# Kernel optimization log

Hardware: AMD Instinct MI355X
Metric: run time of the kernel (lower is better)

The kernel has to match this reference:

```python
import jax, jax.numpy as jnp
import numpy as np

INPUT_SIZE = 128
OUTPUT_SIZE = 32
LIFTING_DIM = 512
BATCH = 32768


def setup_inputs() -> dict:
    key = jax.random.key(0)
    ks = jax.random.split(key, 7)
    x = jax.random.normal(ks[0], (BATCH, INPUT_SIZE), dtype=jnp.float32)
    # Linear(input_size, lifting_dim) with bias (torch layout: W [out, in])
    lim1 = 1.0 / np.sqrt(INPUT_SIZE)
    W1 = jax.random.uniform(ks[1], (LIFTING_DIM, INPUT_SIZE), jnp.float32, -lim1, lim1)
    b1 = jax.random.uniform(ks[2], (LIFTING_DIM,), jnp.float32, -lim1, lim1)
    # Linear(lifting_dim, output_size, bias=False)
    lim2 = 1.0 / np.sqrt(LIFTING_DIM)
    W2 = jax.random.uniform(ks[3], (OUTPUT_SIZE, LIFTING_DIM), jnp.float32, -lim2, lim2)
    # Quadratic params: L_vars ~ randn, b ~ randn, c ~ randn (as in module init)
    n_tril = LIFTING_DIM * (LIFTING_DIM + 1) // 2
    L_vars = jax.random.normal(ks[4], (n_tril,), dtype=jnp.float32)
    qb = jax.random.normal(ks[5], (LIFTING_DIM,), dtype=jnp.float32)
    qc = jax.random.normal(ks[6], (1,), dtype=jnp.float32)
    return {"x": x, "W1": W1, "b1": b1, "W2": W2, "L_vars": L_vars, "qb": qb, "qc": qc}


def reference(x, W1, b1, W2, L_vars, qb, qc):
    # lifting: phi = tanh(x @ W1^T + b1)   [B, lifting_dim]
    phi = jnp.tanh(x @ W1.T + b1)
    # actor: linear feedback (no bias)     [B, output_size]
    pi = phi @ W2.T
    # critic: quadratic form y = phi' Q phi + b' phi + c with Q = L L^T (PSD)
    rows, cols = jnp.tril_indices(LIFTING_DIM)  # row-major, same order as torch.tril_indices
    L = jnp.zeros((LIFTING_DIM, LIFTING_DIM), dtype=L_vars.dtype).at[rows, cols].set(L_vars)
    Q = L @ L.T
    # diag(phi @ Q @ phi.T) == sum((phi @ Q) * phi, axis=1)  -- O(B*d^2), same math
    y = jnp.sum((phi @ Q) * phi, axis=1) + phi @ qb + qc  # [B]
    vf = y[:, None]  # [B, 1]
    return pi, vf
```

## Files before the change

### kernel.cpp

```cpp
#include <hip/hip_runtime.h>
#include <hip/hip_bf16.h>
#include <stdint.h>

typedef short bf16x8 __attribute__((ext_vector_type(8)));
typedef float f32x4 __attribute__((ext_vector_type(4)));

#define DEVI static __device__ __forceinline__

constexpr int B_   = 32768;
constexpr int IN_  = 128;
constexpr int LF_  = 512;
constexpr int OUT_ = 32;

constexpr size_t OFF_LTF = 0;
constexpr size_t OFF_W1F = 524288;
constexpr size_t OFF_W2F = OFF_W1F + 131072;

DEVI short f2bs(float f) { __hip_bfloat16 h = __float2bfloat16(f); return *(short*)&h; }

DEVI float tanh_fast(float v) {
    float e = __expf(2.0f * v);
    return 1.0f - 2.0f * __builtin_amdgcn_rcpf(e + 1.0f);
}

DEVI bf16x8 fragGL(const __hip_bfloat16* base, int chunk, int ln) {
    return *(const bf16x8*)(base + ((size_t)chunk * 64 + ln) * 8);
}

DEVI bf16x8 phiFrag(const char* p, int row, int kofs) {
    int c = (kofs >> 3) ^ (row & 7);
    return *(const bf16x8*)(p + (size_t)((row << 6) + c) * 16);
}
DEVI bf16x8 xFrag(const char* p, int row, int kofs) {
    int c = (kofs >> 3) ^ (row & 15);
    return *(const bf16x8*)(p + (size_t)((row << 4) + c) * 16);
}

__global__ __launch_bounds__(256) void k_prep(
        const float* __restrict__ w1, const float* __restrict__ w2,
        const float* __restrict__ lv, const float* __restrict__ qb,
        __hip_bfloat16* __restrict__ w1f, __hip_bfloat16* __restrict__ w2f,
        __hip_bfloat16* __restrict__ ltf) {
    int cid = blockIdx.x * 256 + threadIdx.x;
    if (cid < 8192) {
        int ln = cid & 63, ks = (cid >> 6) & 3, nt = cid >> 8;
        int n = nt * 16 + (ln & 15), kb = ks * 32 + (ln >> 4) * 8;
        const float* src = w1 + (size_t)n * IN_ + kb;
        bf16x8 o;
#pragma unroll
        for (int i = 0; i < 8; ++i) o[i] = f2bs(src[i]);
        *(bf16x8*)(w1f + (size_t)cid * 8) = o;
    } else if (cid < 11264) {
        int c2 = cid - 8192;
        int ln = c2 & 63, ks = (c2 >> 6) & 15, nt = c2 >> 10;
        int n = nt * 16 + (ln & 15), kb = ks * 32 + (ln >> 4) * 8;
        bf16x8 o;
#pragma unroll
        for (int i = 0; i < 8; ++i) {
            float v = (n < OUT_) ? w2[(size_t)n * LF_ + kb + i]
                                 : (n == OUT_ ? qb[kb + i] : 0.f);
            o[i] = f2bs(v);
        }
        *(bf16x8*)(w2f + (size_t)c2 * 8) = o;
    } else if (cid < 44032) {
        int c3 = cid - 11264;
        int ln = c3 & 63, ks = (c3 >> 6) & 15, t = c3 >> 10;
        int j = t * 16 + (ln & 15), kb = ks * 32 + (ln >> 4) * 8;
        bf16x8 o;
#pragma unroll
        for (int i = 0; i < 8; ++i) {
            int k = kb + i;
            o[i] = (k >= j) ? f2bs(lv[(size_t)k * (k + 1) / 2 + j]) : (short)0;
        }
        *(bf16x8*)(ltf + (size_t)c3 * 8) = o;
    }
}

__global__ __launch_bounds__(512, 4) void k_fused(
        const float* __restrict__ x, const __hip_bfloat16* __restrict__ w1f,
        const float* __restrict__ b1, const __hip_bfloat16* __restrict__ w2f,
        const __hip_bfloat16* __restrict__ ltf, const float* __restrict__ qcp,
        float* __restrict__ pi, float* __restrict__ vf) {
    __shared__ char smem[81920];
    char*  phiB  = smem;
    char*  stage = smem + 65536;
    float* vfb   = (float*)stage;
    float* vfp   = (float*)(stage + 256);

    const int tid = threadIdx.x, wv = tid >> 6, ln = tid & 63;
    const int cl = ln & 15, q = ln >> 4;
    const int m0 = blockIdx.x * 64;

#pragma unroll
    for (int it = 0; it < 2; ++it) {
        int slot = it * 512 + tid, row = slot >> 4, cg = slot & 15;
        const float4* p = (const float4*)(x + (size_t)(m0 + row) * IN_ + cg * 8);
        float4 u0 = p[0], u1 = p[1];
        bf16x8 pk;
        pk[0] = f2bs(u0.x); pk[1] = f2bs(u0.y); pk[2] = f2bs(u0.z); pk[3] = f2bs(u0.w);
        pk[4] = f2bs(u1.x); pk[5] = f2bs(u1.y); pk[6] = f2bs(u1.z); pk[7] = f2bs(u1.w);
        *(bf16x8*)(stage + (size_t)((row << 4) + (cg ^ (row & 15))) * 16) = pk;
    }
    __syncthreads();

    {
        f32x4 acc[4][4] = {};
        bf16x8 wfr[4], wnx[4];
#pragma unroll
        for (int ni = 0; ni < 4; ++ni) wfr[ni] = fragGL(w1f, (4 * wv + ni) * 4, ln);
#pragma unroll
        for (int ks = 0; ks < 4; ++ks) {
            bf16x8 a[4];
#pragma unroll
            for (int mi = 0; mi < 4; ++mi) a[mi] = xFrag(stage, mi * 16 + cl, ks * 32 + q * 8);
            if (ks < 3)
#pragma unroll
                for (int ni = 0; ni < 4; ++ni)
                    wnx[ni] = fragGL(w1f, (4 * wv + ni) * 4 + ks + 1, ln);
#pragma unroll
            for (int ni = 0; ni < 4; ++ni)
#pragma unroll
                for (int mi = 0; mi < 4; ++mi)
                    acc[ni][mi] = __builtin_amdgcn_mfma_f32_16x16x32_bf16(
                        wfr[ni], a[mi], acc[ni][mi], 0, 0, 0);
#pragma unroll
            for (int ni = 0; ni < 4; ++ni) wfr[ni] = wnx[ni];
        }
#pragma unroll
        for (int ni = 0; ni < 4; ++ni) {
            float4 bb = *(const float4*)(b1 + wv * 64 + ni * 16 + q * 4);
            int c0 = wv * 8 + ni * 2 + (q >> 1);
#pragma unroll
            for (int mi = 0; mi < 4; ++mi) {
                int row = mi * 16 + cl;
                short4 pk;
                pk.x = f2bs(tanh_fast(acc[ni][mi][0] + bb.x));
                pk.y = f2bs(tanh_fast(acc[ni][mi][1] + bb.y));
                pk.z = f2bs(tanh_fast(acc[ni][mi][2] + bb.z));
                pk.w = f2bs(tanh_fast(acc[ni][mi][3] + bb.w));
                *(short4*)(phiB + (size_t)((row << 6) + (c0 ^ (row & 7))) * 16
                           + (q & 1) * 8) = pk;
            }
        }
    }
    __syncthreads();

    {
        int ids[2] = { (wv < 4) ? 2 * wv : 8 + (wv - 4), (wv < 4) ? 2 * wv + 1 : -1 };
#pragma unroll
        for (int u = 0; u < 2; ++u) {
            int id = ids[u];
            if (id < 0) continue;
            int mi = id & 3, ni = id >> 2;
            f32x4 a2 = {};
#pragma unroll
            for (int ks = 0; ks < 16; ++ks) {
                bf16x8 a = phiFrag(phiB, mi * 16 + cl, ks * 32 + q * 8);
                bf16x8 b = fragGL(w2f, ni * 16 + ks, ln);
                a2 = __builtin_amdgcn_mfma_f32_16x16x32_bf16(a, b, a2, 0, 0, 0);
            }
#pragma unroll
            for (int r = 0; r < 4; ++r) {
                int row = mi * 16 + q * 4 + r, col = ni * 16 + cl;
                if (col < OUT_)       pi[(size_t)(m0 + row) * OUT_ + col] = a2[r];
                else if (col == OUT_) vfb[row] = a2[r];
            }
        }
    }

    {
        const int tl[4] = { wv, 15 - wv, 16 + wv, 31 - wv };
        int kstart[4];
#pragma unroll
        for (int j = 0; j < 4; ++j) kstart[j] = (tl[j] * 16) & ~31;
        const int kmin = kstart[0];
        f32x4 acc[4][4] = {};
        bf16x8 b[4];
#pragma unroll
        for (int j = 0; j < 4; ++j)
            if (kmin >= kstart[j]) b[j] = fragGL(ltf, tl[j] * 16 + (kmin >> 5), ln);
        for (int k0 = kmin; k0 < LF_; k0 += 32) {
            int k1 = k0 + 32;
            bf16x8 a[4];
#pragma unroll
            for (int mi = 0; mi < 4; ++mi) a[mi] = phiFrag(phiB, mi * 16 + cl, k0 + q * 8);
            bf16x8 bn[4];
            if (k1 < LF_) {
                int ks1 = k1 >> 5;
#pragma unroll
                for (int j = 0; j < 4; ++j)
                    if (k1 >= kstart[j]) bn[j] = fragGL(ltf, tl[j] * 16 + ks1, ln);
            }
#pragma unroll
            for (int j = 0; j < 4; ++j) {
                if (k0 >= kstart[j]) {
#pragma unroll
                    for (int mi = 0; mi < 4; ++mi)
                        acc[j][mi] = __builtin_amdgcn_mfma_f32_16x16x32_bf16(
                            a[mi], b[j], acc[j][mi], 0, 0, 0);
                }
            }
#pragma unroll
            for (int j = 0; j < 4; ++j) b[j] = bn[j];
        }
#pragma unroll
        for (int mi = 0; mi < 4; ++mi)
#pragma unroll
            for (int r = 0; r < 4; ++r) {
                float s = 0.f;
#pragma unroll
                for (int j = 0; j < 4; ++j) { float t = acc[j][mi][r]; s += t * t; }
                s += __shfl_xor(s, 1, 64);
                s += __shfl_xor(s, 2, 64);
                s += __shfl_xor(s, 4, 64);
                s += __shfl_xor(s, 8, 64);
                if (cl == 0) vfp[wv * 64 + mi * 16 + q * 4 + r] = s;
            }
    }
    __syncthreads();
    if (tid < 64) {
        float v = vfb[tid] + qcp[0];
#pragma unroll
        for (int w = 0; w < 8; ++w) v += vfp[w * 64 + tid];
        vf[m0 + tid] = v;
    }
}

extern "C" void kernel_launch(void* const* d_in, const int* in_sizes, int n_in,
                              void* d_out, int out_size, void* d_ws, size_t ws_size,
                              hipStream_t stream) {
    const float* x  = (const float*)d_in[0];
    const float* w1 = (const float*)d_in[1];
    const float* b1 = (const float*)d_in[2];
    const float* w2 = (const float*)d_in[3];
    const float* lv = (const float*)d_in[4];
    const float* qb = (const float*)d_in[5];
    const float* qc = (const float*)d_in[6];

    char* ws = (char*)d_ws;
    __hip_bfloat16* ltf = (__hip_bfloat16*)(ws + OFF_LTF);
    __hip_bfloat16* w1f = (__hip_bfloat16*)(ws + OFF_W1F);
    __hip_bfloat16* w2f = (__hip_bfloat16*)(ws + OFF_W2F);

    float* pi = (float*)d_out;
    float* vf = pi + (size_t)B_ * OUT_;

    k_prep <<<172, 256, 0, stream>>>(w1, w2, lv, qb, w1f, w2f, ltf);
    k_fused<<<B_ / 64, 512, 0, stream>>>(x, w1f, b1, w2f, ltf, qc, pi, vf);
}
```

Measured before the change: 108.6 us.

## Switch quadratic-form GEMM to 32x32x16 MFMA with per-wave templated triangular loops

The L-factor GEMM in the critic path now uses 32x32x16 bf16 MFMA tiles instead of 16x16x32. Each wave takes two 32-column tiles of L, paired so the triangular work is balanced, and runs fully unrolled compile-time loops chosen through a switch on the wave index. The L prep layout is reworked to match the 32-wide fragments, and the reduction shuffles widen to 32 lanes. The register prefetch of W1 fragments in the first GEMM is also dropped in favour of loading them inside each k-step, which may expose global load latency.

```diff
diff --git a/kernel.cpp b/kernel.cpp
--- a/kernel.cpp
+++ b/kernel.cpp
@@ -4,6 +4,7 @@
 
 typedef short bf16x8 __attribute__((ext_vector_type(8)));
 typedef float f32x4 __attribute__((ext_vector_type(4)));
+typedef float f32x16 __attribute__((ext_vector_type(16)));
 
 #define DEVI static __device__ __forceinline__
 
@@ -26,14 +27,47 @@
 DEVI bf16x8 fragGL(const __hip_bfloat16* base, int chunk, int ln) {
     return *(const bf16x8*)(base + ((size_t)chunk * 64 + ln) * 8);
 }
+DEVI f32x16 mfma32(bf16x8 a, bf16x8 b, f32x16 c) {
+    return __builtin_amdgcn_mfma_f32_32x32x16_bf16(a, b, c, 0, 0, 0);
+}
 
 DEVI bf16x8 phiFrag(const char* p, int row, int kofs) {
     int c = (kofs >> 3) ^ (row & 7);
     return *(const bf16x8*)(p + (size_t)((row << 6) + c) * 16);
 }
+DEVI bf16x8 phiFrag32(const char* p, int h, int ks, int ln) {
+    int row = h * 32 + (ln & 31);
+    int c = (ks * 2 + (ln >> 5)) ^ (row & 7);
+    return *(const bf16x8*)(p + (size_t)((row << 6) + c) * 16);
+}
 DEVI bf16x8 xFrag(const char* p, int row, int kofs) {
     int c = (kofs >> 3) ^ (row & 15);
     return *(const bf16x8*)(p + (size_t)((row << 4) + c) * 16);
+}
+
+template <int WV>
+DEVI void p3loops(const char* phiB, const __hip_bfloat16* ltf, int ln,
+                  f32x16 acc[2][2]) {
+    constexpr int T1 = 15 - WV;
+#pragma unroll
+    for (int ks = 2 * WV; ks < 2 * T1; ++ks) {
+        bf16x8 b0 = fragGL(ltf, WV * 32 + ks, ln);
+        bf16x8 a0 = phiFrag32(phiB, 0, ks, ln);
+        bf16x8 a1 = phiFrag32(phiB, 1, ks, ln);
+        acc[0][0] = mfma32(a0, b0, acc[0][0]);
+        acc[0][1] = mfma32(a1, b0, acc[0][1]);
+    }
+#pragma unroll
+    for (int ks = 2 * T1; ks < 32; ++ks) {
+        bf16x8 b0 = fragGL(ltf, WV * 32 + ks, ln);
+        bf16x8 b1 = fragGL(ltf, T1 * 32 + ks, ln);
+        bf16x8 a0 = phiFrag32(phiB, 0, ks, ln);
+        bf16x8 a1 = phiFrag32(phiB, 1, ks, ln);
+        acc[0][0] = mfma32(a0, b0, acc[0][0]);
+        acc[0][1] = mfma32(a1, b0, acc[0][1]);
+        acc[1][0] = mfma32(a0, b1, acc[1][0]);
+        acc[1][1] = mfma32(a1, b1, acc[1][1]);
+    }
 }
 
 __global__ __launch_bounds__(256) void k_prep(
@@ -64,13 +98,13 @@
         *(bf16x8*)(w2f + (size_t)c2 * 8) = o;
     } else if (cid < 44032) {
         int c3 = cid - 11264;
-        int ln = c3 & 63, ks = (c3 >> 6) & 15, t = c3 >> 10;
-        int j = t * 16 + (ln & 15), kb = ks * 32 + (ln >> 4) * 8;
+        int ln = c3 & 63, ks = (c3 >> 6) & 31, t = c3 >> 11;
+        int n = t * 32 + (ln & 31), kb = ks * 16 + (ln >> 5) * 8;
         bf16x8 o;
 #pragma unroll
         for (int i = 0; i < 8; ++i) {
             int k = kb + i;
-            o[i] = (k >= j) ? f2bs(lv[(size_t)k * (k + 1) / 2 + j]) : (short)0;
+            o[i] = (k >= n) ? f2bs(lv[(size_t)k * (k + 1) / 2 + n]) : (short)0;
         }
         *(bf16x8*)(ltf + (size_t)c3 * 8) = o;
     }
@@ -105,26 +139,19 @@
 
     {
         f32x4 acc[4][4] = {};
-        bf16x8 wfr[4], wnx[4];
-#pragma unroll
-        for (int ni = 0; ni < 4; ++ni) wfr[ni] = fragGL(w1f, (4 * wv + ni) * 4, ln);
 #pragma unroll
         for (int ks = 0; ks < 4; ++ks) {
-            bf16x8 a[4];
+            bf16x8 a[4], wfr[4];
 #pragma unroll
             for (int mi = 0; mi < 4; ++mi) a[mi] = xFrag(stage, mi * 16 + cl, ks * 32 + q * 8);
-            if (ks < 3)
-#pragma unroll
-                for (int ni = 0; ni < 4; ++ni)
-                    wnx[ni] = fragGL(w1f, (4 * wv + ni) * 4 + ks + 1, ln);
+#pragma unroll
+            for (int ni = 0; ni < 4; ++ni) wfr[ni] = fragGL(w1f, (4 * wv + ni) * 4 + ks, ln);
 #pragma unroll
             for (int ni = 0; ni < 4; ++ni)
 #pragma unroll
                 for (int mi = 0; mi < 4; ++mi)
                     acc[ni][mi] = __builtin_amdgcn_mfma_f32_16x16x32_bf16(
                         wfr[ni], a[mi], acc[ni][mi], 0, 0, 0);
-#pragma unroll
-            for (int ni = 0; ni < 4; ++ni) wfr[ni] = wnx[ni];
         }
 #pragma unroll
         for (int ni = 0; ni < 4; ++ni) {
@@ -169,52 +196,30 @@
     }
 
     {
-        const int tl[4] = { wv, 15 - wv, 16 + wv, 31 - wv };
-        int kstart[4];
-#pragma unroll
-        for (int j = 0; j < 4; ++j) kstart[j] = (tl[j] * 16) & ~31;
-        const int kmin = kstart[0];
-        f32x4 acc[4][4] = {};
-        bf16x8 b[4];
-#pragma unroll
-        for (int j = 0; j < 4; ++j)
-            if (kmin >= kstart[j]) b[j] = fragGL(ltf, tl[j] * 16 + (kmin >> 5), ln);
-        for (int k0 = kmin; k0 < LF_; k0 += 32) {
-            int k1 = k0 + 32;
-            bf16x8 a[4];
-#pragma unroll
-            for (int mi = 0; mi < 4; ++mi) a[mi] = phiFrag(phiB, mi * 16 + cl, k0 + q * 8);
-            bf16x8 bn[4];
-            if (k1 < LF_) {
-                int ks1 = k1 >> 5;
-#pragma unroll
-                for (int j = 0; j < 4; ++j)
-                    if (k1 >= kstart[j]) bn[j] = fragGL(ltf, tl[j] * 16 + ks1, ln);
-            }
-#pragma unroll
-            for (int j = 0; j < 4; ++j) {
-                if (k0 >= kstart[j]) {
-#pragma unroll
-                    for (int mi = 0; mi < 4; ++mi)
-                        acc[j][mi] = __builtin_amdgcn_mfma_f32_16x16x32_bf16(
-                            a[mi], b[j], acc[j][mi], 0, 0, 0);
-                }
-            }
-#pragma unroll
-            for (int j = 0; j < 4; ++j) b[j] = bn[j];
-        }
-#pragma unroll
-        for (int mi = 0; mi < 4; ++mi)
-#pragma unroll
-            for (int r = 0; r < 4; ++r) {
-                float s = 0.f;
-#pragma unroll
-                for (int j = 0; j < 4; ++j) { float t = acc[j][mi][r]; s += t * t; }
+        f32x16 acc[2][2] = {};
+        switch (wv) {
+            case 0: p3loops<0>(phiB, ltf, ln, acc); break;
+            case 1: p3loops<1>(phiB, ltf, ln, acc); break;
+            case 2: p3loops<2>(phiB, ltf, ln, acc); break;
+            case 3: p3loops<3>(phiB, ltf, ln, acc); break;
+            case 4: p3loops<4>(phiB, ltf, ln, acc); break;
+            case 5: p3loops<5>(phiB, ltf, ln, acc); break;
+            case 6: p3loops<6>(phiB, ltf, ln, acc); break;
+            default: p3loops<7>(phiB, ltf, ln, acc); break;
+        }
+#pragma unroll
+        for (int h = 0; h < 2; ++h)
+#pragma unroll
+            for (int r = 0; r < 16; ++r) {
+                float t0 = acc[0][h][r], t1 = acc[1][h][r];
+                float s = t0 * t0 + t1 * t1;
                 s += __shfl_xor(s, 1, 64);
                 s += __shfl_xor(s, 2, 64);
                 s += __shfl_xor(s, 4, 64);
                 s += __shfl_xor(s, 8, 64);
-                if (cl == 0) vfp[wv * 64 + mi * 16 + q * 4 + r] = s;
+                s += __shfl_xor(s, 16, 64);
+                if ((ln & 31) == 0)
+                    vfp[wv * 64 + h * 32 + (r & 3) + 8 * (r >> 2) + 4 * (ln >> 5)] = s;
             }
     }
     __syncthreads();
```

Result: no change. 108.7 us (+0.1%).

## Use slab-based phi LDS layout, drop register prefetch, reorder actor after critic

Applied to the files above, without the earlier changes.

Phi is now stored in shared memory in a per-slab chunked layout that matches the MFMA fragment order, replacing the XOR-swizzled row layout, so fragment loads become contiguous 16-byte slot accesses. The explicit double-buffered global prefetch of W1 and L fragments is removed in favour of direct loads inside the loop, which lowers register pressure but relies on the compiler and occupancy to hide latency. The actor (W2) matmul is moved after the critic quadratic-form stage.

```diff
diff --git a/kernel.cpp b/kernel.cpp
--- a/kernel.cpp
+++ b/kernel.cpp
@@ -26,14 +26,18 @@
 DEVI bf16x8 fragGL(const __hip_bfloat16* base, int chunk, int ln) {
     return *(const bf16x8*)(base + ((size_t)chunk * 64 + ln) * 8);
 }
-
-DEVI bf16x8 phiFrag(const char* p, int row, int kofs) {
-    int c = (kofs >> 3) ^ (row & 7);
-    return *(const bf16x8*)(p + (size_t)((row << 6) + c) * 16);
-}
+DEVI f32x4 mfma16(bf16x8 a, bf16x8 b, f32x4 c) {
+    return __builtin_amdgcn_mfma_f32_16x16x32_bf16(a, b, c, 0, 0, 0);
+}
+
 DEVI bf16x8 xFrag(const char* p, int row, int kofs) {
     int c = (kofs >> 3) ^ (row & 15);
     return *(const bf16x8*)(p + (size_t)((row << 4) + c) * 16);
+}
+DEVI bf16x8 phi16s(const char* slab, int mi, int ksl, int cl, int q) {
+    int chunk = ksl * 4 + (q >> 1) * 2 + (mi >> 1);
+    int slot  = (mi & 1) * 16 + cl + 32 * (q & 1);
+    return *(const bf16x8*)(slab + ((size_t)chunk * 64 + slot) * 16);
 }
 
 __global__ __launch_bounds__(256) void k_prep(
@@ -82,7 +86,7 @@
         const __hip_bfloat16* __restrict__ ltf, const float* __restrict__ qcp,
         float* __restrict__ pi, float* __restrict__ vf) {
     __shared__ char smem[81920];
-    char*  phiB  = smem;
+    char*  phiS  = smem;
     char*  stage = smem + 65536;
     float* vfb   = (float*)stage;
     float* vfp   = (float*)(stage + 256);
@@ -105,68 +109,39 @@
 
     {
         f32x4 acc[4][4] = {};
-        bf16x8 wfr[4], wnx[4];
-#pragma unroll
-        for (int ni = 0; ni < 4; ++ni) wfr[ni] = fragGL(w1f, (4 * wv + ni) * 4, ln);
 #pragma unroll
         for (int ks = 0; ks < 4; ++ks) {
-            bf16x8 a[4];
+            bf16x8 a[4], wfr[4];
 #pragma unroll
             for (int mi = 0; mi < 4; ++mi) a[mi] = xFrag(stage, mi * 16 + cl, ks * 32 + q * 8);
-            if (ks < 3)
-#pragma unroll
-                for (int ni = 0; ni < 4; ++ni)
-                    wnx[ni] = fragGL(w1f, (4 * wv + ni) * 4 + ks + 1, ln);
+#pragma unroll
+            for (int ni = 0; ni < 4; ++ni) wfr[ni] = fragGL(w1f, (4 * wv + ni) * 4 + ks, ln);
 #pragma unroll
             for (int ni = 0; ni < 4; ++ni)
 #pragma unroll
                 for (int mi = 0; mi < 4; ++mi)
                     acc[ni][mi] = __builtin_amdgcn_mfma_f32_16x16x32_bf16(
                         wfr[ni], a[mi], acc[ni][mi], 0, 0, 0);
-#pragma unroll
-            for (int ni = 0; ni < 4; ++ni) wfr[ni] = wnx[ni];
-        }
+        }
+        char* slab = phiS + (size_t)(wv >> 1) * 16384;
 #pragma unroll
         for (int ni = 0; ni < 4; ++ni) {
             float4 bb = *(const float4*)(b1 + wv * 64 + ni * 16 + q * 4);
-            int c0 = wv * 8 + ni * 2 + (q >> 1);
+            int chunk = (wv & 1) * 8 + ni * 2;
 #pragma unroll
             for (int mi = 0; mi < 4; ++mi) {
-                int row = mi * 16 + cl;
                 short4 pk;
                 pk.x = f2bs(tanh_fast(acc[ni][mi][0] + bb.x));
                 pk.y = f2bs(tanh_fast(acc[ni][mi][1] + bb.y));
                 pk.z = f2bs(tanh_fast(acc[ni][mi][2] + bb.z));
                 pk.w = f2bs(tanh_fast(acc[ni][mi][3] + bb.w));
-                *(short4*)(phiB + (size_t)((row << 6) + (c0 ^ (row & 7))) * 16
+                int slot = (mi & 1) * 16 + cl + 32 * (q >> 1);
+                *(short4*)(slab + ((size_t)(chunk + (mi >> 1)) * 64 + slot) * 16
                            + (q & 1) * 8) = pk;
             }
         }
     }
     __syncthreads();
-
-    {
-        int ids[2] = { (wv < 4) ? 2 * wv : 8 + (wv - 4), (wv < 4) ? 2 * wv + 1 : -1 };
-#pragma unroll
-        for (int u = 0; u < 2; ++u) {
-            int id = ids[u];
-            if (id < 0) continue;
-            int mi = id & 3, ni = id >> 2;
-            f32x4 a2 = {};
-#pragma unroll
-            for (int ks = 0; ks < 16; ++ks) {
-                bf16x8 a = phiFrag(phiB, mi * 16 + cl, ks * 32 + q * 8);
-                bf16x8 b = fragGL(w2f, ni * 16 + ks, ln);
-                a2 = __builtin_amdgcn_mfma_f32_16x16x32_bf16(a, b, a2, 0, 0, 0);
-            }
-#pragma unroll
-            for (int r = 0; r < 4; ++r) {
-                int row = mi * 16 + q * 4 + r, col = ni * 16 + cl;
-                if (col < OUT_)       pi[(size_t)(m0 + row) * OUT_ + col] = a2[r];
-                else if (col == OUT_) vfb[row] = a2[r];
-            }
-        }
-    }
 
     {
         const int tl[4] = { wv, 15 - wv, 16 + wv, 31 - wv };
@@ -175,33 +150,23 @@
         for (int j = 0; j < 4; ++j) kstart[j] = (tl[j] * 16) & ~31;
         const int kmin = kstart[0];
         f32x4 acc[4][4] = {};
-        bf16x8 b[4];
-#pragma unroll
-        for (int j = 0; j < 4; ++j)
-            if (kmin >= kstart[j]) b[j] = fragGL(ltf, tl[j] * 16 + (kmin >> 5), ln);
         for (int k0 = kmin; k0 < LF_; k0 += 32) {
-            int k1 = k0 + 32;
+            int ks = k0 >> 5;
+            const char* slab = phiS + (size_t)(ks >> 2) * 16384;
+            int ksl = ks & 3;
             bf16x8 a[4];
 #pragma unroll
-            for (int mi = 0; mi < 4; ++mi) a[mi] = phiFrag(phiB, mi * 16 + cl, k0 + q * 8);
-            bf16x8 bn[4];
-            if (k1 < LF_) {
-                int ks1 = k1 >> 5;
-#pragma unroll
-                for (int j = 0; j < 4; ++j)
-                    if (k1 >= kstart[j]) bn[j] = fragGL(ltf, tl[j] * 16 + ks1, ln);
-            }
+            for (int mi = 0; mi < 4; ++mi) a[mi] = phi16s(slab, mi, ksl, cl, q);
 #pragma unroll
             for (int j = 0; j < 4; ++j) {
                 if (k0 >= kstart[j]) {
+                    bf16x8 b = fragGL(ltf, tl[j] * 16 + ks, ln);
 #pragma unroll
                     for (int mi = 0; mi < 4; ++mi)
                         acc[j][mi] = __builtin_amdgcn_mfma_f32_16x16x32_bf16(
-                            a[mi], b[j], acc[j][mi], 0, 0, 0);
+                            a[mi], b, acc[j][mi], 0, 0, 0);
                 }
             }
-#pragma unroll
-            for (int j = 0; j < 4; ++j) b[j] = bn[j];
         }
 #pragma unroll
         for (int mi = 0; mi < 4; ++mi)
@@ -216,6 +181,30 @@
                 s += __shfl_xor(s, 8, 64);
                 if (cl == 0) vfp[wv * 64 + mi * 16 + q * 4 + r] = s;
             }
+    }
+
+    {
+        int ids[2] = { (wv < 4) ? 2 * wv : 8 + (wv - 4), (wv < 4) ? 2 * wv + 1 : -1 };
+#pragma unroll
+        for (int u = 0; u < 2; ++u) {
+            int id = ids[u];
+            if (id < 0) continue;
+            int mi = id & 3, ni = id >> 2;
+            f32x4 a2 = {};
+#pragma unroll
+            for (int ks = 0; ks < 16; ++ks) {
+                const char* slab = phiS + (size_t)(ks >> 2) * 16384;
+                bf16x8 a = phi16s(slab, mi, ks & 3, cl, q);
+                bf16x8 b = fragGL(w2f, ni * 16 + ks, ln);
+                a2 = __builtin_amdgcn_mfma_f32_16x16x32_bf16(a, b, a2, 0, 0, 0);
+            }
+#pragma unroll
+            for (int r = 0; r < 4; ++r) {
+                int row = mi * 16 + q * 4 + r, col = ni * 16 + cl;
+                if (col < OUT_)       pi[(size_t)(m0 + row) * OUT_ + col] = a2[r];
+                else if (col == OUT_) vfb[row] = a2[r];
+            }
+        }
     }
     __syncthreads();
     if (tid < 64) {
```

Result: slower. 111.0 us (+2.2%).
